# Kernel tuning notes

Hardware: AMD Instinct MI355X
Metric: run time of the kernel (lower is better)

Reference implementation:

```python
import jax, jax.numpy as jnp
import numpy as np

R_MAX = 6.0        # BesselBasis r_max (apax default scale)
NUM_RADIAL = 16    # BesselBasis num basis functions
MAX_Z = 119        # chemical embedding vocab
NUM_FEATURES = 128


def _sph_deg3(u):
    """Real spherical harmonics (Racah normalization, Y_00=1) of unit vectors u [E,3],
    degrees 0..3 -> 16 components, m ordered -l..l per degree."""
    x, y, z = u[..., 0], u[..., 1], u[..., 2]
    s3, s15, s10_4, s6_4, s15_2 = jnp.sqrt(3.0), jnp.sqrt(15.0), jnp.sqrt(10.0) / 4, jnp.sqrt(6.0) / 4, jnp.sqrt(15.0) / 2
    x2, y2, z2 = x * x, y * y, z * z
    return jnp.stack([
        jnp.ones_like(x),                     # l=0
        y, z, x,                              # l=1
        s3 * x * y, s3 * y * z, 0.5 * (3 * z2 - 1.0), s3 * x * z, 0.5 * s3 * (x2 - y2),  # l=2
        s10_4 * y * (3 * x2 - y2), s15 * x * y * z, s6_4 * y * (5 * z2 - 1.0),
        0.5 * z * (5 * z2 - 3.0), s6_4 * x * (5 * z2 - 1.0), s15_2 * z * (x2 - y2),
        s10_4 * x * (x2 - 3 * y2),            # l=3
    ], axis=-1)


def setup_inputs() -> dict:
    key = jax.random.key(0)
    k1, k2, k3, k4 = jax.random.split(key, 4)
    E, N = 1_600_000, 50_000
    dr_vec = jax.random.normal(k1, (E, 3), jnp.float32)
    Z = jax.random.randint(k2, (N,), 0, MAX_Z, jnp.int32)
    idx = jax.random.randint(k3, (2, E), 0, N, jnp.int32)
    emb_table = jax.random.normal(k4, (MAX_Z, NUM_FEATURES), jnp.float32) * 0.02
    return {"dr_vec": dr_vec, "Z": Z, "idx": idx, "emb_table": emb_table}


def reference(dr_vec, Z, idx, emb_table):
    N = Z.shape[0]
    i, j = idx[0], idx[1]
    pair_mask = (i != j).astype(dr_vec.dtype)            # [E]
    node_mask = (Z != 0).astype(dr_vec.dtype)            # [N]

    # chemical embedding (gather), masked
    scalar_features = emb_table[Z] * node_mask[:, None]  # [N,F]

    # distances, cosine cutoff, masking
    r = jnp.linalg.norm(dr_vec, axis=-1)                 # [E]
    cutoffs = 0.5 * (jnp.cos(jnp.pi * r / R_MAX) + 1.0) * (r < R_MAX).astype(dr_vec.dtype)
    cutoffs = cutoffs * pair_mask

    # neighborhood size per node, scattered back to edges
    nbh = jax.ops.segment_sum(cutoffs, i, num_segments=N)[i]      # [E]
    pair_scale = jnp.where(pair_mask > 0, 1.0 / jnp.where(nbh > 0, nbh, 1.0), 0.0)

    # Bessel radial basis: sqrt(2/rmax) * sin(n*pi*r/rmax)/r, n=1..NUM_RADIAL
    n = jnp.arange(1, NUM_RADIAL + 1, dtype=dr_vec.dtype)
    safe_r = jnp.where(r > 1e-12, r, 1e-12)[:, None]
    radial_expansion = jnp.sqrt(2.0 / R_MAX) * jnp.sin(n * jnp.pi * safe_r / R_MAX) / safe_r
    radial_expansion = radial_expansion * cutoffs[:, None]        # [E,16]

    # spherical harmonics of unit displacement, scaled, scatter-aggregated
    u = dr_vec / safe_r
    spherical_expansion = _sph_deg3(u) * pair_scale[:, None]      # [E,16]
    spherical_features = jax.ops.segment_sum(spherical_expansion, i, num_segments=N)
    spherical_features = spherical_features * node_mask[:, None]  # [N,16]

    # aggregate radial expansion too so the full gather-compute-scatter chain is live
    radial_features = jax.ops.segment_sum(radial_expansion, i, num_segments=N) * node_mask[:, None]

    # num_layers=0: return all produced node features concatenated [N, 128+16+16]
    return jnp.concatenate([scalar_features, spherical_features, radial_features], axis=-1)
```

## Files before the change

### kernel.cpp

```cpp
#include <hip/hip_runtime.h>

#define P1_T 1024
#define P1_K 8
#define MAXB 1024
#define CCAP 2560
#define P2_T 256

__device__ __forceinline__ float i2f(int b) { return __int_as_float(b); }

__global__ void k_bin2(const int* __restrict__ idx, const float* __restrict__ dr,
                       int* __restrict__ ccnt, int* __restrict__ bucket,
                       int E, int nbk) {
    __shared__ int s_hist[MAXB];
    __shared__ int s_base[MAXB];
    __shared__ int s_cur[MAXB];
    int tid = threadIdx.x;
    for (int b = tid; b < nbk; b += P1_T) { s_hist[b] = 0; s_cur[b] = 0; }
    __syncthreads();
    long long base = (long long)blockIdx.x * (P1_T * P1_K);
    for (int k = 0; k < P1_K; k++) {
        long long e = base + k * P1_T + tid;
        if (e < E) atomicAdd(&s_hist[idx[e] >> 6], 1);
    }
    __syncthreads();
    for (int b = tid; b < nbk; b += P1_T) {
        int h = s_hist[b];
        s_base[b] = (h > 0) ? atomicAdd(&ccnt[b], h) : 0;
    }
    __syncthreads();
    for (int k = 0; k < P1_K; k++) {
        long long e = base + k * P1_T + tid;
        if (e < E) {
            int i = idx[e];
            int j = idx[E + e];
            int b = i >> 6;
            int p = s_base[b] + atomicAdd(&s_cur[b], 1);
            if (p < CCAP) {
                int xb = __float_as_int(dr[3 * e + 0]);
                int yb = __float_as_int(dr[3 * e + 1]);
                int zb = __float_as_int(dr[3 * e + 2]);
                int li = (i == j) ? 64 : (i & 63);
                int w = (zb & 0xFFFFFF80) | li;
                int* o = bucket + ((long long)b * CCAP + p) * 3;
                o[0] = xb; o[1] = yb; o[2] = w;
            }
        }
    }
}

__global__ void k_node4(const int* __restrict__ Z,
                        const int* __restrict__ ccnt,
                        const int* __restrict__ bucket,
                        const float* __restrict__ emb,
                        float* __restrict__ out, int N) {
    __shared__ int s_sx[CCAP];
    __shared__ int s_sy[CCAP];
    __shared__ int s_sz[CCAP];
    __shared__ int s_hist[64];
    __shared__ int s_start[64];
    __shared__ int s_cur[64];

    int g = blockIdx.x;
    int tid = threadIdx.x;
    int node0 = g << 6;
    int cnt = ccnt[g];
    if (cnt > CCAP) cnt = CCAP;
    const int* bk = bucket + (long long)g * CCAP * 3;

    if (tid < 64) s_hist[tid] = 0;
    __syncthreads();

    for (int t = tid; t < cnt; t += P2_T) {
        int li = bk[3 * t + 2] & 127;
        if (li < 64) atomicAdd(&s_hist[li], 1);
    }
    __syncthreads();

    if (tid < 64) {
        int lane = tid;
        int h = s_hist[lane];
        int v = h;
#pragma unroll
        for (int d = 1; d < 64; d <<= 1) {
            int u = __shfl_up(v, d);
            if (lane >= d) v += u;
        }
        s_start[lane] = v - h;
        s_cur[lane] = v - h;
    }
    __syncthreads();

    for (int t = tid; t < cnt; t += P2_T) {
        int xb = bk[3 * t + 0];
        int yb = bk[3 * t + 1];
        int w  = bk[3 * t + 2];
        int li = w & 127;
        if (li < 64) {
            int pos = atomicAdd(&s_cur[li], 1);
            s_sx[pos] = xb;
            s_sy[pos] = yb;
            s_sz[pos] = w & 0xFFFFFF80;
        }
    }
    __syncthreads();

    const float s3   = 1.7320508075688772f;
    const float s15  = 3.872983346207417f;
    const float s104 = 0.7905694150420949f;
    const float s64c = 0.6123724356957945f;
    const float s152 = 1.936491673103709f;

    int wave = tid >> 6;
    int lane = tid & 63;
    int group = lane >> 3;
    int sub = lane & 7;

    for (int round = 0; round < 2; round++) {
        int li = (round << 5) + (wave << 3) + group;
        int n = node0 + li;
        int st = s_start[li];
        int deg = s_hist[li];

        float acc[33];
#pragma unroll
        for (int k = 0; k < 33; k++) acc[k] = 0.0f;

        for (int p = sub; p < deg; p += 8) {
            float x = i2f(s_sx[st + p]);
            float y = i2f(s_sy[st + p]);
            float z = i2f(s_sz[st + p]);
            float r = sqrtf(x * x + y * y + z * z);
            float rs = fmaxf(r, 1e-12f);
            float inv_r = 1.0f / rs;
            float s, c;
            __sincosf(0.5235987755982988f * rs, &s, &c);
            float cut = (r < 6.0f) ? (0.5f * (c + 1.0f)) : 0.0f;
            acc[32] += cut;

            float ux = x * inv_r, uy = y * inv_r, uz = z * inv_r;
            float x2 = ux * ux, y2 = uy * uy, z2 = uz * uz;

            acc[0] += 1.0f;
            acc[1] += uy;
            acc[2] += uz;
            acc[3] += ux;
            acc[4] += s3 * ux * uy;
            acc[5] += s3 * uy * uz;
            acc[6] += 0.5f * (3.0f * z2 - 1.0f);
            acc[7] += s3 * ux * uz;
            acc[8] += 0.5f * s3 * (x2 - y2);
            acc[9] += s104 * uy * (3.0f * x2 - y2);
            acc[10] += s15 * ux * uy * uz;
            acc[11] += s64c * uy * (5.0f * z2 - 1.0f);
            acc[12] += 0.5f * uz * (5.0f * z2 - 3.0f);
            acc[13] += s64c * ux * (5.0f * z2 - 1.0f);
            acc[14] += s152 * uz * (x2 - y2);
            acc[15] += s104 * ux * (x2 - 3.0f * y2);

            float coef = 0.5773502691896258f * inv_r * cut;
            float twoc = 2.0f * c;
            float sp = 0.0f, sn = s;
#pragma unroll
            for (int nn = 0; nn < 16; nn++) {
                acc[16 + nn] += coef * sn;
                float nx = twoc * sn - sp;
                sp = sn; sn = nx;
            }
        }

#pragma unroll
        for (int k = 0; k < 33; k++) {
            float v = acc[k];
            v += __shfl_xor(v, 4);
            v += __shfl_xor(v, 2);
            v += __shfl_xor(v, 1);
            acc[k] = v;
        }

        if (sub == 0 && n < N) {
            float zmask = (Z[n] != 0) ? 1.0f : 0.0f;
            float nbh = acc[32];
            float ps = (nbh > 0.0f) ? (1.0f / nbh) : 1.0f;
            float sphs = ps * zmask;
            float4* o4 = (float4*)(out + (long long)n * 160);
#pragma unroll
            for (int q = 0; q < 4; q++) {
                o4[32 + q] = make_float4(acc[4 * q] * sphs, acc[4 * q + 1] * sphs,
                                         acc[4 * q + 2] * sphs, acc[4 * q + 3] * sphs);
            }
#pragma unroll
            for (int q = 0; q < 4; q++) {
                o4[36 + q] = make_float4(acc[16 + 4 * q] * zmask, acc[17 + 4 * q] * zmask,
                                         acc[18 + 4 * q] * zmask, acc[19 + 4 * q] * zmask);
            }
        }
    }

    for (int t = tid; t < 64 * 32; t += P2_T) {
        int li = t >> 5;
        int q = t & 31;
        int n = node0 + li;
        if (n < N) {
            int zn = Z[n];
            float4 v = make_float4(0.f, 0.f, 0.f, 0.f);
            if (zn != 0) v = ((const float4*)emb)[(long long)zn * 32 + q];
            ((float4*)out)[(long long)n * 40 + q] = v;
        }
    }
}

extern "C" void kernel_launch(void* const* d_in, const int* in_sizes, int n_in,
                              void* d_out, int out_size, void* d_ws, size_t ws_size,
                              hipStream_t stream) {
    const float* dr = (const float*)d_in[0];
    const int* Z = (const int*)d_in[1];
    const int* idx = (const int*)d_in[2];
    const float* emb = (const float*)d_in[3];
    float* out = (float*)d_out;

    int E = in_sizes[0] / 3;
    int N = in_sizes[1];
    int nbk = (N + 63) >> 6;

    int* ccnt = (int*)d_ws;
    int* bucket = ccnt + MAXB;

    hipMemsetAsync(ccnt, 0, (size_t)MAXB * sizeof(int), stream);

    int g1 = (E + P1_T * P1_K - 1) / (P1_T * P1_K);
    k_bin2<<<g1, P1_T, 0, stream>>>(idx, dr, ccnt, bucket, E, nbk);

    k_node4<<<nbk, P2_T, 0, stream>>>(Z, ccnt, bucket, emb, out, N);
}
```

Baseline: 142.3 us.

## Vectorize binning loads, store bucket entries as int4, load node buckets once into registers

The binning kernel now gives each thread 8 contiguous edges and reads idx and dr with int4/float4 loads instead of strided scalar loads. Each binned edge is written as one 16-byte int4 record (x, y, z, local index), so z is no longer packed into low mantissa bits. The node kernel reads its bucket once into registers and reuses those values for both the histogram and scatter passes instead of reading global memory twice. The costs are a 33% larger bucket footprint, more register pressure from the per-thread arrays, and less coalesced per-thread access patterns in binning.

```diff
diff --git a/kernel.cpp b/kernel.cpp
--- a/kernel.cpp
+++ b/kernel.cpp
@@ -1,15 +1,16 @@
 #include <hip/hip_runtime.h>
 
-#define P1_T 1024
-#define P1_K 8
+#define P1_T 512
+#define P1_E 8
 #define MAXB 1024
 #define CCAP 2560
 #define P2_T 256
+#define P2_C ((CCAP + P2_T - 1) / P2_T)
 
 __device__ __forceinline__ float i2f(int b) { return __int_as_float(b); }
 
-__global__ void k_bin2(const int* __restrict__ idx, const float* __restrict__ dr,
-                       int* __restrict__ ccnt, int* __restrict__ bucket,
+__global__ void k_bin3(const int* __restrict__ idx, const float* __restrict__ dr,
+                       int* __restrict__ ccnt, int4* __restrict__ bucket,
                        int E, int nbk) {
     __shared__ int s_hist[MAXB];
     __shared__ int s_base[MAXB];
@@ -17,45 +18,80 @@
     int tid = threadIdx.x;
     for (int b = tid; b < nbk; b += P1_T) { s_hist[b] = 0; s_cur[b] = 0; }
     __syncthreads();
-    long long base = (long long)blockIdx.x * (P1_T * P1_K);
-    for (int k = 0; k < P1_K; k++) {
-        long long e = base + k * P1_T + tid;
-        if (e < E) atomicAdd(&s_hist[idx[e] >> 6], 1);
-    }
-    __syncthreads();
+
+    long long e0 = (long long)blockIdx.x * (P1_T * P1_E) + (long long)tid * P1_E;
+    bool full = (e0 + P1_E <= E);
+
+    int iv[P1_E];
+    if (full) {
+        int4 a = *(const int4*)(idx + e0);
+        int4 b = *(const int4*)(idx + e0 + 4);
+        iv[0] = a.x; iv[1] = a.y; iv[2] = a.z; iv[3] = a.w;
+        iv[4] = b.x; iv[5] = b.y; iv[6] = b.z; iv[7] = b.w;
+    } else {
+#pragma unroll
+        for (int k = 0; k < P1_E; k++) iv[k] = (e0 + k < E) ? idx[e0 + k] : -1;
+    }
+#pragma unroll
+    for (int k = 0; k < P1_E; k++)
+        if (iv[k] >= 0) atomicAdd(&s_hist[iv[k] >> 6], 1);
+    __syncthreads();
+
     for (int b = tid; b < nbk; b += P1_T) {
         int h = s_hist[b];
         s_base[b] = (h > 0) ? atomicAdd(&ccnt[b], h) : 0;
     }
     __syncthreads();
-    for (int k = 0; k < P1_K; k++) {
-        long long e = base + k * P1_T + tid;
-        if (e < E) {
-            int i = idx[e];
-            int j = idx[E + e];
-            int b = i >> 6;
+
+    int jv[P1_E];
+    float f[3 * P1_E];
+    if (full) {
+        int4 a = *(const int4*)(idx + E + e0);
+        int4 b = *(const int4*)(idx + E + e0 + 4);
+        jv[0] = a.x; jv[1] = a.y; jv[2] = a.z; jv[3] = a.w;
+        jv[4] = b.x; jv[5] = b.y; jv[6] = b.z; jv[7] = b.w;
+        const float4* dp = (const float4*)(dr + 3 * e0);
+#pragma unroll
+        for (int q = 0; q < 6; q++) {
+            float4 v = dp[q];
+            f[4 * q + 0] = v.x; f[4 * q + 1] = v.y;
+            f[4 * q + 2] = v.z; f[4 * q + 3] = v.w;
+        }
+    } else {
+#pragma unroll
+        for (int k = 0; k < P1_E; k++) {
+            if (e0 + k < E) {
+                jv[k] = idx[E + e0 + k];
+                f[3 * k + 0] = dr[3 * (e0 + k) + 0];
+                f[3 * k + 1] = dr[3 * (e0 + k) + 1];
+                f[3 * k + 2] = dr[3 * (e0 + k) + 2];
+            } else jv[k] = -1;
+        }
+    }
+#pragma unroll
+    for (int k = 0; k < P1_E; k++) {
+        if (iv[k] >= 0) {
+            int b = iv[k] >> 6;
             int p = s_base[b] + atomicAdd(&s_cur[b], 1);
             if (p < CCAP) {
-                int xb = __float_as_int(dr[3 * e + 0]);
-                int yb = __float_as_int(dr[3 * e + 1]);
-                int zb = __float_as_int(dr[3 * e + 2]);
-                int li = (i == j) ? 64 : (i & 63);
-                int w = (zb & 0xFFFFFF80) | li;
-                int* o = bucket + ((long long)b * CCAP + p) * 3;
-                o[0] = xb; o[1] = yb; o[2] = w;
+                int li = (iv[k] == jv[k]) ? 64 : (iv[k] & 63);
+                bucket[(long long)b * CCAP + p] =
+                    make_int4(__float_as_int(f[3 * k + 0]),
+                              __float_as_int(f[3 * k + 1]),
+                              __float_as_int(f[3 * k + 2]), li);
             }
         }
     }
 }
 
-__global__ void k_node4(const int* __restrict__ Z,
+__global__ void k_node5(const int* __restrict__ Z,
                         const int* __restrict__ ccnt,
-                        const int* __restrict__ bucket,
+                        const int4* __restrict__ bucket,
                         const float* __restrict__ emb,
                         float* __restrict__ out, int N) {
-    __shared__ int s_sx[CCAP];
-    __shared__ int s_sy[CCAP];
-    __shared__ int s_sz[CCAP];
+    __shared__ float s_sx[CCAP];
+    __shared__ float s_sy[CCAP];
+    __shared__ float s_sz[CCAP];
     __shared__ int s_hist[64];
     __shared__ int s_start[64];
     __shared__ int s_cur[64];
@@ -65,41 +101,45 @@
     int node0 = g << 6;
     int cnt = ccnt[g];
     if (cnt > CCAP) cnt = CCAP;
-    const int* bk = bucket + (long long)g * CCAP * 3;
+    const int4* bk = bucket + (long long)g * CCAP;
 
     if (tid < 64) s_hist[tid] = 0;
     __syncthreads();
 
-    for (int t = tid; t < cnt; t += P2_T) {
-        int li = bk[3 * t + 2] & 127;
-        if (li < 64) atomicAdd(&s_hist[li], 1);
+    int4 pld[P2_C];
+#pragma unroll
+    for (int c = 0; c < P2_C; c++) {
+        int t = tid + c * P2_T;
+        if (t < cnt) pld[c] = bk[t];
+    }
+#pragma unroll
+    for (int c = 0; c < P2_C; c++) {
+        int t = tid + c * P2_T;
+        if (t < cnt && pld[c].w < 64) atomicAdd(&s_hist[pld[c].w], 1);
     }
     __syncthreads();
 
     if (tid < 64) {
-        int lane = tid;
-        int h = s_hist[lane];
+        int h = s_hist[tid];
         int v = h;
 #pragma unroll
         for (int d = 1; d < 64; d <<= 1) {
             int u = __shfl_up(v, d);
-            if (lane >= d) v += u;
-        }
-        s_start[lane] = v - h;
-        s_cur[lane] = v - h;
-    }
-    __syncthreads();
-
-    for (int t = tid; t < cnt; t += P2_T) {
-        int xb = bk[3 * t + 0];
-        int yb = bk[3 * t + 1];
-        int w  = bk[3 * t + 2];
-        int li = w & 127;
-        if (li < 64) {
-            int pos = atomicAdd(&s_cur[li], 1);
-            s_sx[pos] = xb;
-            s_sy[pos] = yb;
-            s_sz[pos] = w & 0xFFFFFF80;
+            if (tid >= d) v += u;
+        }
+        s_start[tid] = v - h;
+        s_cur[tid] = v - h;
+    }
+    __syncthreads();
+
+#pragma unroll
+    for (int c = 0; c < P2_C; c++) {
+        int t = tid + c * P2_T;
+        if (t < cnt && pld[c].w < 64) {
+            int pos = atomicAdd(&s_cur[pld[c].w], 1);
+            s_sx[pos] = i2f(pld[c].x);
+            s_sy[pos] = i2f(pld[c].y);
+            s_sz[pos] = i2f(pld[c].z);
         }
     }
     __syncthreads();
@@ -126,9 +166,9 @@
         for (int k = 0; k < 33; k++) acc[k] = 0.0f;
 
         for (int p = sub; p < deg; p += 8) {
-            float x = i2f(s_sx[st + p]);
-            float y = i2f(s_sy[st + p]);
-            float z = i2f(s_sz[st + p]);
+            float x = s_sx[st + p];
+            float y = s_sy[st + p];
+            float z = s_sz[st + p];
             float r = sqrtf(x * x + y * y + z * z);
             float rs = fmaxf(r, 1e-12f);
             float inv_r = 1.0f / rs;
@@ -223,12 +263,13 @@
     int nbk = (N + 63) >> 6;
 
     int* ccnt = (int*)d_ws;
-    int* bucket = ccnt + MAXB;
+    int4* bucket = (int4*)(ccnt + MAXB);
 
     hipMemsetAsync(ccnt, 0, (size_t)MAXB * sizeof(int), stream);
 
-    int g1 = (E + P1_T * P1_K - 1) / (P1_T * P1_K);
-    k_bin2<<<g1, P1_T, 0, stream>>>(idx, dr, ccnt, bucket, E, nbk);
-
-    k_node4<<<nbk, P2_T, 0, stream>>>(Z, ccnt, bucket, emb, out, N);
+    long long per_block = (long long)P1_T * P1_E;
+    int g1 = (int)((E + per_block - 1) / per_block);
+    k_bin3<<<g1, P1_T, 0, stream>>>(idx, dr, ccnt, bucket, E, nbk);
+
+    k_node5<<<nbk, P2_T, 0, stream>>>(Z, ccnt, bucket, emb, out, N);
 }
```

After: 134.5 us. 1.06x faster.
